# Performance work log

Measured on AMD Instinct MI355X. Metric: run time of the kernel, lower is better.

## Reference

```python
import jax, jax.numpy as jnp
import numpy as np

FACTOR = 1
EPS = 1e-8
SCALES = (1, 2, 4)


def _pool(x, scale):
    # adaptive_avg_pool1d along time with L % scale == 0 -> uniform bin mean
    if scale == 1:
        return x
    B, L, H, E = x.shape
    return x.reshape(B, L // scale, scale, H, E).mean(axis=2)


def _interp_linear(x, L_out):
    # F.interpolate(mode='linear', align_corners=False) along time axis (axis=1)
    B, Ls, H, E = x.shape
    i = jnp.arange(L_out, dtype=jnp.float32)
    src = jnp.maximum((i + 0.5) * (Ls / L_out) - 0.5, 0.0)
    x0 = jnp.floor(src).astype(jnp.int32)
    x1 = jnp.minimum(x0 + 1, Ls - 1)
    lam = (src - x0.astype(jnp.float32))[None, :, None, None]
    return x[:, x0] * (1.0 - lam) + x[:, x1] * lam


def _corr_agg(q, k, v, w1, b1, w2, b2, w3, b3):
    # q,k,v: [B, Ls, H, E]
    B, Ls, H, E = q.shape
    qf = jnp.fft.rfft(q.transpose(0, 2, 3, 1), axis=-1)   # [B,H,E,Lf]
    kf = jnp.fft.rfft(k.transpose(0, 2, 3, 1), axis=-1)
    corr = jnp.fft.irfft(qf * jnp.conj(kf), n=Ls, axis=-1).astype(jnp.float32)  # [B,H,E,Ls]

    # ---- adaptive-k features ----
    energy = jnp.mean(jnp.sum(corr ** 2, axis=(1, 2)))          # scalar, expanded to B
    var = jnp.var(corr.reshape(B, -1), axis=1, ddof=1)          # unbiased, like torch.var
    cm = corr.reshape(B, H * E, Ls).mean(axis=1)                # [B, Ls]
    pk = jnp.sum((cm[:, 1:-1] > cm[:, :-2]) & (cm[:, 1:-1] > cm[:, 2:]), axis=1).astype(jnp.float32)
    feats = jnp.stack([jnp.broadcast_to(energy, (B,)), var, pk], axis=1)  # [B,3]
    h = jax.nn.relu(feats @ w1.T + b1)
    h = jax.nn.relu(h @ w2.T + b2)
    ratio = jax.nn.sigmoid(h @ w3.T + b3)[:, 0]                 # [B]
    kvals = jnp.clip((ratio * Ls * FACTOR).astype(jnp.int32), 1, Ls)  # [B]

    # ---- adaptive time-delay aggregation ----
    c = corr.transpose(0, 3, 1, 2)                              # [B, Ls, H, E]
    interior = (c[:, 1:-1] > c[:, :-2]) & (c[:, 1:-1] > c[:, 2:])
    pad = jnp.zeros((B, 1, H, E), dtype=bool)
    peaks = jnp.concatenate([pad, interior, pad], axis=1)       # [B,Ls,H,E] local maxima

    neg_inf = jnp.float32(-jnp.inf)
    vals = jnp.where(peaks, c, neg_inf).reshape(B, -1)
    count = peaks.reshape(B, -1).sum(axis=1)
    sorted_desc = -jnp.sort(-vals, axis=1)
    thresh = jnp.take_along_axis(sorted_desc, (kvals - 1)[:, None], axis=1)[:, 0]  # k-th largest peak
    topk_mask = peaks & (c >= thresh[:, None, None, None])
    keep_topk = (count > kvals)[:, None, None, None]
    final = jnp.where(keep_topk, topk_mask, peaks)

    attn = jnp.where(final, c, 0.0)
    w = jax.nn.softmax(attn + EPS, axis=1)                      # softmax over time lags
    return w * v                                                # einsum('lhe,lhe->lhe') == elementwise


def setup_inputs() -> dict:
    key = jax.random.key(0)
    ks = jax.random.split(key, 10)
    B, L, H, E = 16, 1024, 8, 64
    return {
        "queries": jax.random.normal(ks[0], (B, L, H, E), jnp.float32),
        "keys": jax.random.normal(ks[1], (B, L, H, E), jnp.float32),
        "values": jax.random.normal(ks[2], (B, L, H, E), jnp.float32),
        "scale_weights": jax.random.normal(ks[3], (3,), jnp.float32) * 0.1 + 1.0 / 3.0,
        "k_w1": jax.random.normal(ks[4], (32, 3), jnp.float32) * 0.1,
        "k_b1": jax.random.normal(ks[5], (32,), jnp.float32) * 0.1,
        "k_w2": jax.random.normal(ks[6], (16, 32), jnp.float32) * 0.1,
        "k_b2": jax.random.normal(ks[7], (16,), jnp.float32) * 0.1,
        "k_w3": jax.random.normal(ks[8], (1, 16), jnp.float32) * 0.1,
        "k_b3": jax.random.normal(ks[9], (1,), jnp.float32) * 0.1,
    }


def reference(queries, keys, values, scale_weights, k_w1, k_b1, k_w2, k_b2, k_w3, k_b3):
    B, L, H, E = queries.shape
    out = jnp.zeros_like(queries)
    for i, scale in enumerate(SCALES):
        q, k, v = _pool(queries, scale), _pool(keys, scale), _pool(values, scale)
        o = _corr_agg(q, k, v, k_w1, k_b1, k_w2, k_b2, k_w3, k_b3)
        if scale > 1:
            o = _interp_linear(o, L)
        out = out + o * scale_weights[i]
    return out
```

## Files before the change

### kernel.cpp

```cpp
#include <hip/hip_runtime.h>
#include <math.h>

typedef unsigned int u32;
typedef unsigned long long u64;
typedef float f4 __attribute__((ext_vector_type(4)));

#define B_ 16
#define L_ 1024
#define H_ 8
#define E_ 64
#define C_ 512
#define NB_SEL 8
#define GCH 8
#define TC 32
#define CAPR 160
#define CAP1 192
#define KGRP 56

__device__ __forceinline__ size_t co(int sidx) {
  return sidx == 0 ? 0u : (sidx == 1 ? 8388608u : 12582912u);
}
__device__ __forceinline__ u32 pk_off(int sidx) {
  return sidx == 0 ? 0u : (sidx == 1 ? 3211264u : 4816896u);
}
__device__ __forceinline__ u32 pk_cap(int sidx) { return 200704u >> sidx; }

__device__ __forceinline__ u32 f2key(float f) {
  u32 u = __float_as_uint(f);
  return (u & 0x80000000u) ? ~u : (u | 0x80000000u);
}
__device__ __forceinline__ float key2f(u32 k) {
  u32 u = (k & 0x80000000u) ? (k ^ 0x80000000u) : ~k;
  return __uint_as_float(u);
}

__global__ void k_init(u32* histA, u32* histB, u32* peak_cnt, u32* done,
                       double* s1, double* s2, float* cm) {
  const int gid = blockIdx.x * 256 + threadIdx.x;
  const int gs = gridDim.x * 256;
  for (int i = gid; i < 3 * 16 * 256; i += gs) { histA[i] = 0; histB[i] = 0; }
  for (int i = gid; i < 3 * 16 * 1024; i += gs) cm[i] = 0.f;
  for (int i = gid; i < 3 * 16 * 16; i += gs) peak_cnt[i] = 0;
  for (int i = gid; i < 144; i += gs) done[i] = 0;
  for (int i = gid; i < 48; i += gs) { s1[i] = 0.0; s2[i] = 0.0; }
}

__launch_bounds__(512, 4)
__global__ void k_corr1(const float* __restrict__ Q, const float* __restrict__ K,
                        float* __restrict__ corr) {
  constexpr int LS = 1024;
  constexpr int LMASK = LS - 1;
  constexpr int NCHUNK = LS / TC;
  __shared__ __align__(16) float ksT[KGRP * 256];
  __shared__ __align__(16) float qT[2 * 8 * 256];
  const int tid = threadIdx.x;
  const int e = tid & 63;
  const int w = tid >> 6;
  const int slot16 = __builtin_amdgcn_readfirstlane(w << 4);
  const int bh = blockIdx.x;
  const int tau0 = blockIdx.y << 7;
  const int b = bh >> 3, h = bh & 7;
  const size_t gbase = (size_t)b * L_ * C_ + (size_t)h * 64;
  const int e4 = e << 2;
  const int bp0 = 112 - slot16;

  float acc[16];
#pragma unroll
  for (int i = 0; i < 16; ++i) acc[i] = 0.f;

#pragma unroll
  for (int pass = 0; pass < 5; ++pass) {
    const int p0 = pass * 32 + (w << 2);
    f4 v;
#pragma unroll
    for (int j = 0; j < 4; ++j) {
      int tk = (p0 + j - tau0 - 127 + 2048) & LMASK;
      v[j] = K[gbase + (size_t)tk * C_ + e];
    }
    *(f4*)&ksT[(p0 >> 2) * 256 + e4] = v;
    if (p0 < 32) *(f4*)&ksT[((p0 + 192) >> 2) * 256 + e4] = v;
  }
  {
    f4 v;
#pragma unroll
    for (int j = 0; j < 4; ++j)
      v[j] = Q[gbase + (size_t)((w << 2) + j) * C_ + e];
    *(f4*)&qT[w * 256 + e4] = v;
  }
  __syncthreads();

  int cph = 0;
  for (int chunk = 0; chunk < NCHUNK; ++chunk) {
    const int t0 = chunk * TC;
    const bool more = (chunk + 1 < NCHUNK);
    f4 kr, qr;
    int sr = 0;
    if (more) {
      int sp = cph + 160; if (sp >= CAP1) sp -= CAP1;
      sr = sp + (w << 2);
#pragma unroll
      for (int j = 0; j < 4; ++j) {
        int l = t0 + 160 + (w << 2) + j;
        int tk = (l - tau0 - 127 + 2048) & LMASK;
        kr[j] = K[gbase + (size_t)tk * C_ + e];
      }
#pragma unroll
      for (int j = 0; j < 4; ++j)
        qr[j] = Q[gbase + (size_t)(t0 + TC + (w << 2) + j) * C_ + e];
    }
    int bp = bp0 + cph; if (bp >= CAP1) bp -= CAP1;
    const int g0 = bp >> 2;
    f4 km4[12];
#pragma unroll
    for (int j = 0; j < 12; ++j)
      km4[j] = *(const f4*)&ksT[(g0 + j) * 256 + e4];
    const float* qb = qT + (chunk & 1) * 2048;
#pragma unroll
    for (int g = 0; g < 8; ++g) {
      f4 qv = *(const f4*)&qb[g * 256 + e4];
#pragma unroll
      for (int k = 0; k < 4; ++k) {
        const int jt = (g << 2) + k;
#pragma unroll
        for (int i = 0; i < 16; ++i) {
          const int m = 15 + jt - i;
          acc[i] = fmaf(qv[k], km4[m >> 2][m & 3], acc[i]);
        }
      }
    }
    if (more) {
      *(f4*)&ksT[(sr >> 2) * 256 + e4] = kr;
      if (sr < 32) *(f4*)&ksT[((sr + 192) >> 2) * 256 + e4] = kr;
      float* qn = qT + (((chunk & 1) ^ 1)) * 2048;
      *(f4*)&qn[w * 256 + e4] = qr;
    }
    __syncthreads();
    cph += 32; if (cph >= CAP1) cph -= CAP1;
  }
  float* wt = ksT;
#pragma unroll
  for (int i = 0; i < 16; ++i) wt[(slot16 + i) * 65 + e] = acc[i];
  __syncthreads();
  const int to = tid & 127;
  const size_t cbase = ((size_t)b * C_ + (size_t)h * 64) * LS + tau0 + to;
  for (int cr = tid >> 7; cr < 64; cr += 4)
    corr[cbase + (size_t)cr * LS] = wt[to * 65 + cr];
}

template<int S>
__device__ __forceinline__ float4 pool_load(const float* gp) {
  float4 v = *(const float4*)gp;
  if constexpr (S >= 2) {
    float4 v2 = *(const float4*)(gp + C_);
    v.x += v2.x; v.y += v2.y; v.z += v2.z; v.w += v2.w;
  }
  if constexpr (S == 4) {
    float4 v3 = *(const float4*)(gp + 2 * C_);
    float4 v4 = *(const float4*)(gp + 3 * C_);
    v.x += v3.x + v4.x; v.y += v3.y + v4.y;
    v.z += v3.z + v4.z; v.w += v3.w + v4.w;
  }
  constexpr float sc = (S == 1) ? 1.f : (S == 2) ? 0.5f : 0.25f;
  if constexpr (S >= 2) { v.x *= sc; v.y *= sc; v.z *= sc; v.w *= sc; }
  return v;
}

template<int S>
__launch_bounds__(256, 3)
__global__ void k_corr(const float* __restrict__ Q, const float* __restrict__ K,
                       float* __restrict__ corr) {
  constexpr int LS = 1024 / S;
  constexpr int LMASK = LS - 1;
  constexpr int NCHUNK = LS / TC;
  __shared__ float qs[TC * 64];
  __shared__ float ks[CAPR * 64];
  const int tid = threadIdx.x;
  const int e = tid & 63;
  const int slot32 = __builtin_amdgcn_readfirstlane((tid >> 6) << 5);
  const int bh = blockIdx.x;
  const int tau0 = blockIdx.y << 7;
  const int b = bh >> 3, h = bh & 7;
  const size_t gbase = (size_t)b * L_ * C_ + (size_t)h * 64;
  const int l16 = tid & 15;
  const int rbase = tid >> 4;
  const int bp0 = 96 - slot32;

  float acc[32];
#pragma unroll
  for (int i = 0; i < 32; ++i) acc[i] = 0.f;

  int cph = 0;
  for (int chunk = 0; chunk < NCHUNK; ++chunk) {
    const int t0 = chunk * TC;
    __syncthreads();
    {
#pragma unroll
      for (int it = 0; it < 2; ++it) {
        int row = rbase + it * 16;
        int traw = (t0 + row) * S;
        float4 v = pool_load<S>(Q + gbase + (size_t)traw * C_ + l16 * 4);
        *(float4*)(qs + row * 64 + l16 * 4) = v;
      }
      if (chunk == 0) {
#pragma unroll
        for (int it = 0; it < 10; ++it) {
          int l = rbase + it * 16;
          int tk = (l - tau0 - 127 + 2048) & LMASK;
          float4 v = pool_load<S>(K + gbase + (size_t)tk * S * C_ + l16 * 4);
          *(float4*)(ks + l * 64 + l16 * 4) = v;
        }
      } else {
        int sp = cph + 128; if (sp >= CAPR) sp -= CAPR;
#pragma unroll
        for (int it = 0; it < 2; ++it) {
          int row = rbase + it * 16;
          int l = t0 + 128 + row;
          int tk = (l - tau0 - 127 + 2048) & LMASK;
          int p = sp + row; if (p >= CAPR) p -= CAPR;
          float4 v = pool_load<S>(K + gbase + (size_t)tk * S * C_ + l16 * 4);
          *(float4*)(ks + p * 64 + l16 * 4) = v;
        }
      }
      __syncthreads();
    }
    int bp = bp0 + cph; if (bp >= CAPR) bp -= CAPR;
    float km[63];
    if (bp <= CAPR - 47) {
#pragma unroll
      for (int m = 0; m < 47; ++m) km[m] = ks[(bp + m) * 64 + e];
    } else {
#pragma unroll
      for (int m = 0; m < 47; ++m) {
        int p = bp + m; if (p >= CAPR) p -= CAPR;
        km[m] = ks[p * 64 + e];
      }
    }
#pragma unroll
    for (int jt = 0; jt < 16; ++jt) {
      float qv = qs[jt * 64 + e];
#pragma unroll
      for (int i = 0; i < 32; ++i) acc[i] = fmaf(qv, km[31 + jt - i], acc[i]);
    }
    if (bp <= CAPR - 63) {
#pragma unroll
      for (int m = 47; m < 63; ++m) km[m] = ks[(bp + m) * 64 + e];
    } else {
#pragma unroll
      for (int m = 47; m < 63; ++m) {
        int p = bp + m; if (p >= CAPR) p -= CAPR;
        km[m] = ks[p * 64 + e];
      }
    }
#pragma unroll
    for (int jt = 16; jt < 32; ++jt) {
      float qv = qs[jt * 64 + e];
#pragma unroll
      for (int i = 0; i < 32; ++i) acc[i] = fmaf(qv, km[31 + jt - i], acc[i]);
    }
    cph += 32; if (cph >= CAPR) cph -= CAPR;
  }
  __syncthreads();
  float* wt = ks;
#pragma unroll
  for (int i = 0; i < 32; ++i) wt[(slot32 + i) * 65 + e] = acc[i];
  __syncthreads();
  const int to = tid & 127;
  const size_t cbase = ((size_t)b * C_ + (size_t)h * 64) * LS + tau0 + to;
  for (int cr = tid >> 7; cr < 64; cr += 2)
    corr[cbase + (size_t)cr * LS] = wt[to * 65 + cr];
}

__launch_bounds__(256, 4)
__global__ void k_stats(const float* __restrict__ corrbase, float* __restrict__ cm,
                        double* s1, double* s2, u32* peak_cnt, u32* histA,
                        u32* pkbase) {
  __shared__ __align__(16) float rows[GCH * 1024];
  __shared__ u32 hist_s[256];
  __shared__ double red_d[8];
  __shared__ u32 wv[4], wbase[4];
  const int tid = threadIdx.x;
  const int sidx = blockIdx.z;
  const int b = blockIdx.y;
  const int sb = sidx * 16 + b;
  const int Ls = 1024 >> sidx;
  const int c0 = blockIdx.x * GCH;
  const int lane = tid & 63;
  const int wave = tid >> 6;
  hist_s[tid] = 0;
  {
    const float4* src4 =
        (const float4*)(corrbase + co(sidx) + ((size_t)b * C_ + c0) * Ls);
    float4* dst4 = (float4*)rows;
    const int n4 = GCH * Ls / 4;
    for (int i = tid; i < n4; i += 256) dst4[i] = src4[i];
  }
  __syncthreads();
  const int nt = Ls >> 8;
  float cmacc[4] = {0.f, 0.f, 0.f, 0.f};
  double ls1 = 0.0, ls2 = 0.0;
  u32 mycnt = 0;
  for (int g = 0; g < GCH; ++g) {
    const float* row = rows + g * Ls;
    for (int i = 0; i < nt; ++i) {
      int t = tid + (i << 8);
      float v = row[t];
      cmacc[i] += v;
      ls1 += (double)v;
      ls2 += (double)v * (double)v;
      bool pk = (t >= 1) && (t <= Ls - 2) && (v > row[t - 1]) && (v > row[t + 1]);
      if (pk) {
        ++mycnt;
        atomicAdd(&hist_s[f2key(v) >> 24], 1u);
      }
    }
  }
  u32 wc = mycnt;
  for (int off = 32; off; off >>= 1) wc += __shfl_down(wc, off, 64);
  if (lane == 0) wv[wave] = wc;
  __syncthreads();
  if (tid == 0) {
    u32 t = 0;
    for (int w = 0; w < 4; ++w) { wbase[w] = t; t += wv[w]; }
    u32 base = atomicAdd(&peak_cnt[sb * 16], t);
    for (int w = 0; w < 4; ++w) wbase[w] += base;
  }
  __syncthreads();
  const u32 cap = pk_cap(sidx);
  u32* dst_pk = pkbase + pk_off(sidx) + (u32)b * cap;
  u32 off_w = wbase[wave];
  const u64 below = (1ull << lane) - 1ull;
  for (int g = 0; g < GCH; ++g) {
    const float* row = rows + g * Ls;
    for (int i = 0; i < nt; ++i) {
      int t = tid + (i << 8);
      float v = row[t];
      bool pk = (t >= 1) && (t <= Ls - 2) && (v > row[t - 1]) && (v > row[t + 1]);
      u64 mask = __ballot(pk);
      if (pk) {
        u32 idx = off_w + (u32)__popcll(mask & below);
        if (idx < cap) dst_pk[idx] = f2key(v);
      }
      off_w += (u32)__popcll(mask);
    }
  }
  for (int i = 0; i < nt; ++i) {
    int t = tid + (i << 8);
    unsafeAtomicAdd(&cm[sb * 1024 + t], cmacc[i]);
  }
  for (int off = 32; off; off >>= 1) {
    ls1 += __shfl_down(ls1, off, 64);
    ls2 += __shfl_down(ls2, off, 64);
  }
  if (lane == 0) { red_d[wave] = ls1; red_d[4 + wave] = ls2; }
  __syncthreads();
  if (tid == 0) {
    unsafeAtomicAdd(&s1[sb], red_d[0] + red_d[1] + red_d[2] + red_d[3]);
    unsafeAtomicAdd(&s2[sb], red_d[4] + red_d[5] + red_d[6] + red_d[7]);
  }
  if (hist_s[tid]) atomicAdd(&histA[sb * 256 + tid], hist_s[tid]);
}

__global__ void k_mlp(const float* __restrict__ cm, const double* s1,
                      const double* s2, const u32* peak_cnt, const u32* histA,
                      int* rank_s, u32* prefix_s, u32* active, float* thresh,
                      const float* w1, const float* b1, const float* w2,
                      const float* b2, const float* w3, const float* b3) {
  __shared__ float wls[673];
  __shared__ float cmrow[1024];
  __shared__ int red_i[4];
  __shared__ u32 cum[256];
  const int tid = threadIdx.x;
  const int sb = blockIdx.x;
  const int sidx = sb >> 4;
  const int Ls = 1024 >> sidx;
  for (int i = tid; i < 96; i += 256) wls[i] = w1[i];
  for (int i = tid; i < 32; i += 256) wls[96 + i] = b1[i];
  for (int i = tid; i < 512; i += 256) wls[128 + i] = w2[i];
  if (tid < 16) wls[640 + tid] = b2[tid];
  if (tid < 16) wls[656 + tid] = w3[tid];
  if (tid == 0) wls[672] = b3[0];
  for (int i = tid; i < Ls; i += 256) cmrow[i] = cm[sb * 1024 + i];
  __syncthreads();
  int cnt = 0;
  for (int t = 1 + tid; t <= Ls - 2; t += 256) {
    float v = cmrow[t];
    cnt += (v > cmrow[t - 1]) && (v > cmrow[t + 1]);
  }
  for (int off = 32; off; off >>= 1) cnt += __shfl_down(cnt, off, 64);
  if ((tid & 63) == 0) red_i[tid >> 6] = cnt;
  __syncthreads();
  if (tid == 0) {
    double tot = 0.0;
    for (int j = 0; j < 16; ++j) tot += s2[sidx * 16 + j];
    float f0 = (float)(tot / (16.0 * (double)Ls));
    double N = (double)C_ * (double)Ls;
    float f1 = (float)((s2[sb] - s1[sb] * s1[sb] / N) / (N - 1.0));
    float f2 = (float)(red_i[0] + red_i[1] + red_i[2] + red_i[3]);
    float h1[32];
    for (int j = 0; j < 32; ++j)
      h1[j] = fmaxf(0.f, wls[j * 3] * f0 + wls[j * 3 + 1] * f1 + wls[j * 3 + 2] * f2 + wls[96 + j]);
    float h2[16];
    for (int j = 0; j < 16; ++j) {
      float a = wls[640 + j];
      for (int i = 0; i < 32; ++i) a += wls[128 + j * 32 + i] * h1[i];
      h2[j] = fmaxf(0.f, a);
    }
    float z = wls[672];
    for (int i = 0; i < 16; ++i) z += wls[656 + i] * h2[i];
    float ratio = 1.0f / (1.0f + __expf(-z));
    int kv = (int)(ratio * (float)Ls);
    kv = min(max(kv, 1), Ls);
    int cntb = (int)peak_cnt[sb * 16];
    active[sb] = (u32)(cntb > kv);
    thresh[sb] = -INFINITY;
    rank_s[sb] = kv;
    prefix_s[sb] = 0;
  }
  __syncthreads();
  cum[tid] = histA[sb * 256 + tid];
  __syncthreads();
  for (int off = 1; off < 256; off <<= 1) {
    u32 add = (tid + off < 256) ? cum[tid + off] : 0u;
    __syncthreads();
    cum[tid] += add;
    __syncthreads();
  }
  u32 act_b = active[sb];
  u32 r = act_b ? (u32)rank_s[sb] : 0u;
  u32 cc = cum[tid];
  u32 cnext = (tid == 255) ? 0u : cum[tid + 1];
  __syncthreads();
  if (act_b && r > 0 && cc >= r && cnext < r) {
    prefix_s[sb] = (u32)tid << 24;
    rank_s[sb] = (int)(r - cnext);
  }
}

__global__ void k_sel(const u32* __restrict__ pkbase, const u32* peak_cnt,
                      const u32* active, int* rank_s, u32* prefix_s,
                      u32* hist, u32* done, float* thresh, int level) {
  __shared__ u32 hist_s[256];
  __shared__ u32 cum[256];
  __shared__ u32 islast;
  const int tid = threadIdx.x;
  const int sb = blockIdx.x / NB_SEL;
  const int blk = blockIdx.x % NB_SEL;
  const int sidx = sb >> 4;
  hist_s[tid] = 0;
  if (tid == 0) islast = 0;
  __syncthreads();
  const int act = (int)active[sb];
  const u32 cap = pk_cap(sidx);
  u32 cnt = peak_cnt[sb * 16];
  if (cnt > cap) cnt = cap;
  if (act) {
    const u32 pref = prefix_s[sb];
    const int hi_sh = 32 - 8 * level;
    const int b_sh = 24 - 8 * level;
    const u32 lo = (u32)(((u64)cnt * (u64)blk) / NB_SEL);
    const u32 hi = (u32)(((u64)cnt * (u64)(blk + 1)) / NB_SEL);
    const u32* src = pkbase + pk_off(sidx) + (u32)(sb & 15) * cap;
    for (u32 i = lo + tid; i < hi; i += 256) {
      u32 key = src[i];
      if ((key >> hi_sh) == (pref >> hi_sh))
        atomicAdd(&hist_s[(key >> b_sh) & 255u], 1u);
    }
  }
  __syncthreads();
  if (hist_s[tid]) atomicAdd(&hist[sb * 256 + tid], hist_s[tid]);
  __syncthreads();
  if (tid == 0) {
    __threadfence();
    u32 t = atomicAdd(&done[(level - 1) * 48 + sb], 1u);
    if (t == NB_SEL - 1) islast = 1;
  }
  __syncthreads();
  if (!islast) return;
  __threadfence();
  u32 hv = atomicAdd(&hist[sb * 256 + tid], 0u);
  cum[tid] = hv;
  hist[sb * 256 + tid] = 0;
  __syncthreads();
  for (int off = 1; off < 256; off <<= 1) {
    u32 add = (tid + off < 256) ? cum[tid + off] : 0u;
    __syncthreads();
    cum[tid] += add;
    __syncthreads();
  }
  u32 r = act ? (u32)rank_s[sb] : 0u;
  u32 pref2 = act ? prefix_s[sb] : 0u;
  u32 cc = cum[tid];
  u32 cnext = (tid == 255) ? 0u : cum[tid + 1];
  __syncthreads();
  if (act && r > 0 && cc >= r && cnext < r) {
    u32 np = pref2 | ((u32)tid << (24 - 8 * level));
    prefix_s[sb] = np;
    rank_s[sb] = (int)(r - cnext);
    if (level == 3) thresh[sb] = key2f(np);
  }
}

__global__ void k_softstats(const float* __restrict__ corrbase, const float* thresh,
                            float2* __restrict__ mZ) {
  __shared__ float row[1024];
  __shared__ float red_s[8];
  const int tid = threadIdx.x;
  const int bc = blockIdx.x;
  const int sidx = blockIdx.y;
  const int Ls = 1024 >> sidx;
  const float th = thresh[sidx * 16 + (bc >> 9)];
  const float* src = corrbase + co(sidx) + (size_t)bc * Ls;
  for (int t = tid; t < Ls; t += 256) row[t] = src[t];
  __syncthreads();
  float mx = 0.f;
  for (int t = tid; t < Ls; t += 256) {
    float v = row[t];
    bool pk = (t >= 1) && (t <= Ls - 2) && (v > row[t - 1]) && (v > row[t + 1]) && (v >= th);
    if (pk) mx = fmaxf(mx, v);
  }
  for (int off = 32; off; off >>= 1) mx = fmaxf(mx, __shfl_down(mx, off, 64));
  if ((tid & 63) == 0) red_s[tid >> 6] = mx;
  __syncthreads();
  float m = fmaxf(fmaxf(red_s[0], red_s[1]), fmaxf(red_s[2], red_s[3]));
  float zs = 0.f;
  for (int t = tid; t < Ls; t += 256) {
    float v = row[t];
    bool pk = (t >= 1) && (t <= Ls - 2) && (v > row[t - 1]) && (v > row[t + 1]) && (v >= th);
    float a = pk ? v : 0.f;
    zs += __expf(a - m);
  }
  for (int off = 32; off; off >>= 1) zs += __shfl_down(zs, off, 64);
  if ((tid & 63) == 0) red_s[4 + (tid >> 6)] = zs;
  __syncthreads();
  if (tid == 0) {
    float Z = red_s[4] + red_s[5] + red_s[6] + red_s[7];
    mZ[sidx * 8192 + bc] = make_float2(m, 1.0f / Z);
  }
}

__launch_bounds__(256, 4)
__global__ void k_apply(const float* __restrict__ corr, const float* __restrict__ V,
                        const float2* __restrict__ mZ, const float* thresh,
                        float* __restrict__ o, int Ls, int s) {
  __shared__ float ct[64][131];
  __shared__ float m_s[64], rz_s[64];
  const int tid = threadIdx.x;
  const int b = blockIdx.z;
  const int c0 = blockIdx.y << 6;
  const int t0 = blockIdx.x << 7;
  {
    const int row0 = tid >> 7, jc = tid & 127;
    for (int rr = row0; rr < 64; rr += 2) {
      const float* src = corr + ((size_t)b * C_ + c0 + rr) * Ls;
      for (int j = jc; j < 130; j += 128) {
        int t = t0 - 1 + j;
        t = max(0, min(t, Ls - 1));
        ct[rr][j] = src[t];
      }
    }
  }
  if (tid < 64) {
    float2 v = mZ[b * C_ + c0 + tid];
    m_s[tid] = v.x; rz_s[tid] = v.y;
  }
  __syncthreads();
  const float th = thresh[b];
  const int cl = tid & 63, ts = tid >> 6;
  for (int ii = 0; ii < 32; ++ii) {
    int tl = ts + (ii << 2);
    int tg = t0 + tl;
    float vm = ct[cl][tl], vc = ct[cl][tl + 1], vp = ct[cl][tl + 2];
    bool pk = (tg >= 1) && (tg <= Ls - 2) && (vc > vm) && (vc > vp) && (vc >= th);
    float a = pk ? vc : 0.f;
    float w = __expf(a - m_s[cl]) * rz_s[cl];
    size_t vb = ((size_t)b * L_ + (size_t)tg * s) * C_ + c0 + cl;
    float vv;
    if (s == 2) vv = (V[vb] + V[vb + C_]) * 0.5f;
    else vv = ((V[vb] + V[vb + C_]) + (V[vb + 2 * C_] + V[vb + 3 * C_])) * 0.25f;
    o[((size_t)b * Ls + tg) * C_ + c0 + cl] = w * vv;
  }
}

__launch_bounds__(256, 4)
__global__ void k_apply_final(const float* __restrict__ corr, const float* __restrict__ V,
                              const float2* __restrict__ mZ, const float* thresh,
                              const float* __restrict__ o2, const float* __restrict__ o4,
                              const float* __restrict__ sw, float* __restrict__ out) {
  __shared__ float ct[64][131];
  __shared__ float m_s[64], rz_s[64];
  const int Ls = 1024;
  const int tid = threadIdx.x;
  const int b = blockIdx.z;
  const int c0 = blockIdx.y << 6;
  const int t0 = blockIdx.x << 7;
  {
    const int row0 = tid >> 7, jc = tid & 127;
    for (int rr = row0; rr < 64; rr += 2) {
      const float* src = corr + ((size_t)b * C_ + c0 + rr) * Ls;
      for (int j = jc; j < 130; j += 128) {
        int t = t0 - 1 + j;
        t = max(0, min(t, Ls - 1));
        ct[rr][j] = src[t];
      }
    }
  }
  if (tid < 64) {
    float2 v = mZ[b * C_ + c0 + tid];
    m_s[tid] = v.x; rz_s[tid] = v.y;
  }
  __syncthreads();
  const float th = thresh[b];
  const float sw0 = sw[0], sw1 = sw[1], sw2 = sw[2];
  const int cl = tid & 63, ts = tid >> 6;
  for (int ii = 0; ii < 32; ++ii) {
    int tl = ts + (ii << 2);
    int tg = t0 + tl;
    float vm = ct[cl][tl], vc = ct[cl][tl + 1], vp = ct[cl][tl + 2];
    bool pk = (tg >= 1) && (tg <= Ls - 2) && (vc > vm) && (vc > vp) && (vc >= th);
    float a = pk ? vc : 0.f;
    float w = __expf(a - m_s[cl]) * rz_s[cl];
    float v1 = V[((size_t)b * L_ + tg) * C_ + c0 + cl];
    float r = sw0 * w * v1;
    {
      float srcp = fmaxf((tg + 0.5f) * 0.5f - 0.5f, 0.f);
      int x0 = (int)srcp;
      float lam = srcp - (float)x0;
      int x1 = min(x0 + 1, 511);
      const float* p = o2 + (size_t)b * 512 * C_ + c0 + cl;
      r += sw1 * ((1.f - lam) * p[(size_t)x0 * C_] + lam * p[(size_t)x1 * C_]);
    }
    {
      float srcp = fmaxf((tg + 0.5f) * 0.25f - 0.5f, 0.f);
      int x0 = (int)srcp;
      float lam = srcp - (float)x0;
      int x1 = min(x0 + 1, 255);
      const float* p = o4 + (size_t)b * 256 * C_ + c0 + cl;
      r += sw2 * ((1.f - lam) * p[(size_t)x0 * C_] + lam * p[(size_t)x1 * C_]);
    }
    out[((size_t)b * L_ + tg) * C_ + c0 + cl] = r;
  }
}

extern "C" void kernel_launch(void* const* d_in, const int* in_sizes, int n_in,
                              void* d_out, int out_size, void* d_ws, size_t ws_size,
                              hipStream_t stream) {
  const float* Q  = (const float*)d_in[0];
  const float* Kk = (const float*)d_in[1];
  const float* V  = (const float*)d_in[2];
  const float* sw = (const float*)d_in[3];
  const float* w1 = (const float*)d_in[4];
  const float* b1 = (const float*)d_in[5];
  const float* w2 = (const float*)d_in[6];
  const float* b2 = (const float*)d_in[7];
  const float* w3 = (const float*)d_in[8];
  const float* b3 = (const float*)d_in[9];
  float* out = (float*)d_out;

  char* ws = (char*)d_ws;
  size_t p = 0;
  auto alloc = [&](size_t n) { char* r = ws + p; p = (p + n + 255) & ~(size_t)255; return r; };
  float*  corr = (float*)alloc((size_t)(8388608 + 4194304 + 2097152) * 4);
  char*   oreg = alloc((size_t)25165824);
  float*  o2   = (float*)oreg;
  float*  o4   = (float*)(oreg + 16777216);
  u32*    pk   = (u32*)oreg;
  float*  cm       = (float*)alloc(3 * 16 * 1024 * 4);
  float2* mZ       = (float2*)alloc(3 * 16 * 512 * 8);
  double* s1d      = (double*)alloc(48 * 8);
  double* s2d      = (double*)alloc(48 * 8);
  u32*    histA    = (u32*)alloc(3 * 16 * 256 * 4);
  u32*    histB    = (u32*)alloc(3 * 16 * 256 * 4);
  u32*    peak_cnt = (u32*)alloc(3 * 16 * 16 * 4);
  u32*    done     = (u32*)alloc(144 * 4);
  int*    rank_s   = (int*)alloc(48 * 4);
  u32*    prefix_s = (u32*)alloc(48 * 4);
  u32*    active   = (u32*)alloc(48 * 4);
  float*  thresh   = (float*)alloc(48 * 4);

  k_init<<<dim3(16), dim3(256), 0, stream>>>(histA, histB, peak_cnt, done,
                                             s1d, s2d, cm);
  k_corr1<<<dim3(128, 8), dim3(512), 0, stream>>>(Q, Kk, corr);
  k_corr<2><<<dim3(128, 4), dim3(256), 0, stream>>>(Q, Kk, corr + 8388608);
  k_corr<4><<<dim3(128, 2), dim3(256), 0, stream>>>(Q, Kk, corr + 12582912);
  k_stats<<<dim3(C_ / GCH, B_, 3), dim3(256), 0, stream>>>(
      corr, cm, s1d, s2d, peak_cnt, histA, pk);
  k_mlp<<<dim3(48), dim3(256), 0, stream>>>(
      cm, s1d, s2d, peak_cnt, histA, rank_s, prefix_s, active, thresh,
      w1, b1, w2, b2, w3, b3);
  for (int level = 1; level <= 3; ++level)
    k_sel<<<dim3(48 * NB_SEL), dim3(256), 0, stream>>>(
        pk, peak_cnt, active, rank_s, prefix_s, histB, done, thresh, level);
  k_softstats<<<dim3(8192, 3), dim3(256), 0, stream>>>(corr, thresh, mZ);
  k_apply<<<dim3(2, 8, 16), dim3(256), 0, stream>>>(
      corr + 12582912, V, mZ + 2 * 8192, thresh + 32, o4, 256, 4);
  k_apply<<<dim3(4, 8, 16), dim3(256), 0, stream>>>(
      corr + 8388608, V, mZ + 1 * 8192, thresh + 16, o2, 512, 2);
  k_apply_final<<<dim3(8, 8, 16), dim3(256), 0, stream>>>(
      corr, V, mZ, thresh, o2, o4, sw, out);
}
```

Before: 800.7 us.

## Reuse 512-thread corr kernel for pooled scales, merge apply launches, widen selection grid

Templates the scale-1 correlation kernel on the pooling factor, with scalar pooled gathers, so scales 2 and 4 use it in place of the separate 256-thread k_corr. The two k_apply launches for the pooled scales are merged into a single launch that branches on blockIdx.x, and the selection kernel gets four times more blocks per batch. The aim is better occupancy and compute structure for the pooled correlations and fewer small launches. In exchange the pooled loads become scalar and uncoalesced per timestep instead of float4, and the wrap of the Q index is changed with a mask.

```diff
diff --git a/kernel.cpp b/kernel.cpp
--- a/kernel.cpp
+++ b/kernel.cpp
@@ -10,10 +10,9 @@
 #define H_ 8
 #define E_ 64
 #define C_ 512
-#define NB_SEL 8
+#define NB_SEL 32
 #define GCH 8
 #define TC 32
-#define CAPR 160
 #define CAP1 192
 #define KGRP 56
 
@@ -45,10 +44,24 @@
   for (int i = gid; i < 48; i += gs) { s1[i] = 0.0; s2[i] = 0.0; }
 }
 
+template<int S>
+__device__ __forceinline__ float gpool(const float* base, int tk, int e) {
+  float v = base[(size_t)(tk * S) * C_ + e];
+  if constexpr (S >= 2) v += base[(size_t)(tk * S + 1) * C_ + e];
+  if constexpr (S == 4) {
+    v += base[(size_t)(tk * S + 2) * C_ + e];
+    v += base[(size_t)(tk * S + 3) * C_ + e];
+  }
+  constexpr float sc = (S == 1) ? 1.f : (S == 2) ? 0.5f : 0.25f;
+  if constexpr (S >= 2) v *= sc;
+  return v;
+}
+
+template<int S>
 __launch_bounds__(512, 4)
 __global__ void k_corr1(const float* __restrict__ Q, const float* __restrict__ K,
                         float* __restrict__ corr) {
-  constexpr int LS = 1024;
+  constexpr int LS = 1024 / S;
   constexpr int LMASK = LS - 1;
   constexpr int NCHUNK = LS / TC;
   __shared__ __align__(16) float ksT[KGRP * 256];
@@ -61,6 +74,8 @@
   const int tau0 = blockIdx.y << 7;
   const int b = bh >> 3, h = bh & 7;
   const size_t gbase = (size_t)b * L_ * C_ + (size_t)h * 64;
+  const float* Qb = Q + gbase;
+  const float* Kb = K + gbase;
   const int e4 = e << 2;
   const int bp0 = 112 - slot16;
 
@@ -75,7 +90,7 @@
 #pragma unroll
     for (int j = 0; j < 4; ++j) {
       int tk = (p0 + j - tau0 - 127 + 2048) & LMASK;
-      v[j] = K[gbase + (size_t)tk * C_ + e];
+      v[j] = gpool<S>(Kb, tk, e);
     }
     *(f4*)&ksT[(p0 >> 2) * 256 + e4] = v;
     if (p0 < 32) *(f4*)&ksT[((p0 + 192) >> 2) * 256 + e4] = v;
@@ -84,7 +99,7 @@
     f4 v;
 #pragma unroll
     for (int j = 0; j < 4; ++j)
-      v[j] = Q[gbase + (size_t)((w << 2) + j) * C_ + e];
+      v[j] = gpool<S>(Qb, (w << 2) + j, e);
     *(f4*)&qT[w * 256 + e4] = v;
   }
   __syncthreads();
@@ -102,11 +117,11 @@
       for (int j = 0; j < 4; ++j) {
         int l = t0 + 160 + (w << 2) + j;
         int tk = (l - tau0 - 127 + 2048) & LMASK;
-        kr[j] = K[gbase + (size_t)tk * C_ + e];
+        kr[j] = gpool<S>(Kb, tk, e);
       }
 #pragma unroll
       for (int j = 0; j < 4; ++j)
-        qr[j] = Q[gbase + (size_t)(t0 + TC + (w << 2) + j) * C_ + e];
+        qr[j] = gpool<S>(Qb, (t0 + TC + (w << 2) + j) & LMASK, e);
     }
     int bp = bp0 + cph; if (bp >= CAP1) bp -= CAP1;
     const int g0 = bp >> 2;
@@ -144,129 +159,6 @@
   const int to = tid & 127;
   const size_t cbase = ((size_t)b * C_ + (size_t)h * 64) * LS + tau0 + to;
   for (int cr = tid >> 7; cr < 64; cr += 4)
-    corr[cbase + (size_t)cr * LS] = wt[to * 65 + cr];
-}
-
-template<int S>
-__device__ __forceinline__ float4 pool_load(const float* gp) {
-  float4 v = *(const float4*)gp;
-  if constexpr (S >= 2) {
-    float4 v2 = *(const float4*)(gp + C_);
-    v.x += v2.x; v.y += v2.y; v.z += v2.z; v.w += v2.w;
-  }
-  if constexpr (S == 4) {
-    float4 v3 = *(const float4*)(gp + 2 * C_);
-    float4 v4 = *(const float4*)(gp + 3 * C_);
-    v.x += v3.x + v4.x; v.y += v3.y + v4.y;
-    v.z += v3.z + v4.z; v.w += v3.w + v4.w;
-  }
-  constexpr float sc = (S == 1) ? 1.f : (S == 2) ? 0.5f : 0.25f;
-  if constexpr (S >= 2) { v.x *= sc; v.y *= sc; v.z *= sc; v.w *= sc; }
-  return v;
-}
-
-template<int S>
-__launch_bounds__(256, 3)
-__global__ void k_corr(const float* __restrict__ Q, const float* __restrict__ K,
-                       float* __restrict__ corr) {
-  constexpr int LS = 1024 / S;
-  constexpr int LMASK = LS - 1;
-  constexpr int NCHUNK = LS / TC;
-  __shared__ float qs[TC * 64];
-  __shared__ float ks[CAPR * 64];
-  const int tid = threadIdx.x;
-  const int e = tid & 63;
-  const int slot32 = __builtin_amdgcn_readfirstlane((tid >> 6) << 5);
-  const int bh = blockIdx.x;
-  const int tau0 = blockIdx.y << 7;
-  const int b = bh >> 3, h = bh & 7;
-  const size_t gbase = (size_t)b * L_ * C_ + (size_t)h * 64;
-  const int l16 = tid & 15;
-  const int rbase = tid >> 4;
-  const int bp0 = 96 - slot32;
-
-  float acc[32];
-#pragma unroll
-  for (int i = 0; i < 32; ++i) acc[i] = 0.f;
-
-  int cph = 0;
-  for (int chunk = 0; chunk < NCHUNK; ++chunk) {
-    const int t0 = chunk * TC;
-    __syncthreads();
-    {
-#pragma unroll
-      for (int it = 0; it < 2; ++it) {
-        int row = rbase + it * 16;
-        int traw = (t0 + row) * S;
-        float4 v = pool_load<S>(Q + gbase + (size_t)traw * C_ + l16 * 4);
-        *(float4*)(qs + row * 64 + l16 * 4) = v;
-      }
-      if (chunk == 0) {
-#pragma unroll
-        for (int it = 0; it < 10; ++it) {
-          int l = rbase + it * 16;
-          int tk = (l - tau0 - 127 + 2048) & LMASK;
-          float4 v = pool_load<S>(K + gbase + (size_t)tk * S * C_ + l16 * 4);
-          *(float4*)(ks + l * 64 + l16 * 4) = v;
-        }
-      } else {
-        int sp = cph + 128; if (sp >= CAPR) sp -= CAPR;
-#pragma unroll
-        for (int it = 0; it < 2; ++it) {
-          int row = rbase + it * 16;
-          int l = t0 + 128 + row;
-          int tk = (l - tau0 - 127 + 2048) & LMASK;
-          int p = sp + row; if (p >= CAPR) p -= CAPR;
-          float4 v = pool_load<S>(K + gbase + (size_t)tk * S * C_ + l16 * 4);
-          *(float4*)(ks + p * 64 + l16 * 4) = v;
-        }
-      }
-      __syncthreads();
-    }
-    int bp = bp0 + cph; if (bp >= CAPR) bp -= CAPR;
-    float km[63];
-    if (bp <= CAPR - 47) {
-#pragma unroll
-      for (int m = 0; m < 47; ++m) km[m] = ks[(bp + m) * 64 + e];
-    } else {
-#pragma unroll
-      for (int m = 0; m < 47; ++m) {
-        int p = bp + m; if (p >= CAPR) p -= CAPR;
-        km[m] = ks[p * 64 + e];
-      }
-    }
-#pragma unroll
-    for (int jt = 0; jt < 16; ++jt) {
-      float qv = qs[jt * 64 + e];
-#pragma unroll
-      for (int i = 0; i < 32; ++i) acc[i] = fmaf(qv, km[31 + jt - i], acc[i]);
-    }
-    if (bp <= CAPR - 63) {
-#pragma unroll
-      for (int m = 47; m < 63; ++m) km[m] = ks[(bp + m) * 64 + e];
-    } else {
-#pragma unroll
-      for (int m = 47; m < 63; ++m) {
-        int p = bp + m; if (p >= CAPR) p -= CAPR;
-        km[m] = ks[p * 64 + e];
-      }
-    }
-#pragma unroll
-    for (int jt = 16; jt < 32; ++jt) {
-      float qv = qs[jt * 64 + e];
-#pragma unroll
-      for (int i = 0; i < 32; ++i) acc[i] = fmaf(qv, km[31 + jt - i], acc[i]);
-    }
-    cph += 32; if (cph >= CAPR) cph -= CAPR;
-  }
-  __syncthreads();
-  float* wt = ks;
-#pragma unroll
-  for (int i = 0; i < 32; ++i) wt[(slot32 + i) * 65 + e] = acc[i];
-  __syncthreads();
-  const int to = tid & 127;
-  const size_t cbase = ((size_t)b * C_ + (size_t)h * 64) * LS + tau0 + to;
-  for (int cr = tid >> 7; cr < 64; cr += 2)
     corr[cbase + (size_t)cr * LS] = wt[to * 65 + cr];
 }
 
@@ -539,15 +431,25 @@
 }
 
 __launch_bounds__(256, 4)
-__global__ void k_apply(const float* __restrict__ corr, const float* __restrict__ V,
-                        const float2* __restrict__ mZ, const float* thresh,
-                        float* __restrict__ o, int Ls, int s) {
+__global__ void k_apply2(const float* __restrict__ corr2c, const float* __restrict__ corr4c,
+                         const float* __restrict__ V,
+                         const float2* __restrict__ mZ2, const float2* __restrict__ mZ4,
+                         const float* __restrict__ th2, const float* __restrict__ th4,
+                         float* __restrict__ o2p, float* __restrict__ o4p) {
   __shared__ float ct[64][131];
   __shared__ float m_s[64], rz_s[64];
   const int tid = threadIdx.x;
   const int b = blockIdx.z;
   const int c0 = blockIdx.y << 6;
-  const int t0 = blockIdx.x << 7;
+  const int xb = blockIdx.x;
+  const int is4 = (xb < 2);
+  const int s = is4 ? 4 : 2;
+  const int Ls = is4 ? 256 : 512;
+  const int t0 = (is4 ? xb : (xb - 2)) << 7;
+  const float* corr = is4 ? corr4c : corr2c;
+  const float2* mZ = is4 ? mZ4 : mZ2;
+  const float* thp = is4 ? th4 : th2;
+  float* o = is4 ? o4p : o2p;
   {
     const int row0 = tid >> 7, jc = tid & 127;
     for (int rr = row0; rr < 64; rr += 2) {
@@ -564,7 +466,7 @@
     m_s[tid] = v.x; rz_s[tid] = v.y;
   }
   __syncthreads();
-  const float th = thresh[b];
+  const float th = thp[b];
   const int cl = tid & 63, ts = tid >> 6;
   for (int ii = 0; ii < 32; ++ii) {
     int tl = ts + (ii << 2);
@@ -679,9 +581,9 @@
 
   k_init<<<dim3(16), dim3(256), 0, stream>>>(histA, histB, peak_cnt, done,
                                              s1d, s2d, cm);
-  k_corr1<<<dim3(128, 8), dim3(512), 0, stream>>>(Q, Kk, corr);
-  k_corr<2><<<dim3(128, 4), dim3(256), 0, stream>>>(Q, Kk, corr + 8388608);
-  k_corr<4><<<dim3(128, 2), dim3(256), 0, stream>>>(Q, Kk, corr + 12582912);
+  k_corr1<1><<<dim3(128, 8), dim3(512), 0, stream>>>(Q, Kk, corr);
+  k_corr1<2><<<dim3(128, 4), dim3(512), 0, stream>>>(Q, Kk, corr + 8388608);
+  k_corr1<4><<<dim3(128, 2), dim3(512), 0, stream>>>(Q, Kk, corr + 12582912);
   k_stats<<<dim3(C_ / GCH, B_, 3), dim3(256), 0, stream>>>(
       corr, cm, s1d, s2d, peak_cnt, histA, pk);
   k_mlp<<<dim3(48), dim3(256), 0, stream>>>(
@@ -691,10 +593,9 @@
     k_sel<<<dim3(48 * NB_SEL), dim3(256), 0, stream>>>(
         pk, peak_cnt, active, rank_s, prefix_s, histB, done, thresh, level);
   k_softstats<<<dim3(8192, 3), dim3(256), 0, stream>>>(corr, thresh, mZ);
-  k_apply<<<dim3(2, 8, 16), dim3(256), 0, stream>>>(
-      corr + 12582912, V, mZ + 2 * 8192, thresh + 32, o4, 256, 4);
-  k_apply<<<dim3(4, 8, 16), dim3(256), 0, stream>>>(
-      corr + 8388608, V, mZ + 1 * 8192, thresh + 16, o2, 512, 2);
+  k_apply2<<<dim3(6, 8, 16), dim3(256), 0, stream>>>(
+      corr + 8388608, corr + 12582912, V, mZ + 8192, mZ + 2 * 8192,
+      thresh + 16, thresh + 32, o2, o4);
   k_apply_final<<<dim3(8, 8, 16), dim3(256), 0, stream>>>(
       corr, V, mZ, thresh, o2, o4, sw, out);
 }
```

New measurement: 764.2 us. -4.6%, faster.
